# Optimization experiments

Measured on AMD Instinct MI355X. Metric: run time of the kernel, lower is better.

## Reference

```python
import jax, jax.numpy as jnp
import numpy as np

T, K, F = 131072, 64, 8
EPS = 1e-10


def setup_inputs() -> dict:
    key = jax.random.key(0)
    k0, k1, k2, k3 = jax.random.split(key, 4)
    return {
        "observations": jax.random.normal(k0, (T, F), dtype=jnp.float32),
        "beta_logits": jax.random.normal(k1, (K,), dtype=jnp.float32),
        "pi_logits": jax.random.normal(k2, (K, K), dtype=jnp.float32),
        "means": 0.1 * jax.random.normal(k3, (K, F), dtype=jnp.float32),
        "log_vars": jnp.zeros((K, F), dtype=jnp.float32),
    }


def _stick_breaking(logits):
    betas = jax.nn.sigmoid(logits)
    cp = jnp.cumprod(1.0 - betas)
    return betas * jnp.concatenate([jnp.ones((1,), betas.dtype), cp[:-1]])


def _emission_log_probs(obs, means, log_vars):
    # Diagonal-covariance MVN log-prob, vectorized over (T, K) via matmuls
    # logN(x; mu, diag(v)) = -0.5 * (sum((x-mu)^2/v) + sum(log v) + F*log(2pi))
    inv_var = jnp.exp(-log_vars)                                 # (K, F)
    quad = (obs ** 2) @ inv_var.T                                # (T, K): sum x^2/v
    cross = obs @ (means * inv_var).T                            # (T, K): sum x*mu/v
    const = jnp.sum(means ** 2 * inv_var + log_vars, axis=1)     # (K,)
    log2pi = jnp.float32(np.log(2.0 * np.pi))
    Fdim = obs.shape[1]
    return -0.5 * (quad - 2.0 * cross + const[None, :] + Fdim * log2pi)


def reference(observations, beta_logits, pi_logits, means, log_vars):
    beta_w = _stick_breaking(beta_logits)                        # (K,)
    trans = jax.nn.softmax(pi_logits, axis=1)                    # (K, K)
    em = jnp.exp(_emission_log_probs(observations, means, log_vars))  # (T, K)

    # Forward recursion
    a0 = beta_w * em[0]
    a0 = a0 / (a0.sum() + EPS)

    def fwd_step(a, e):
        a = (a @ trans) * e
        a = a / (a.sum() + EPS)
        return a, a

    _, alpha_rest = jax.lax.scan(fwd_step, a0, em[1:])
    alpha = jnp.concatenate([a0[None, :], alpha_rest], axis=0)   # (T, K)

    # Backward recursion: beta[t] = normalize(trans @ (beta[t+1] * em[t+1]))
    bT = jnp.ones((trans.shape[0],), observations.dtype)

    def bwd_step(b, e_next):
        b = trans @ (b * e_next)
        b = b / (b.sum() + EPS)
        return b, b

    _, beta_rev = jax.lax.scan(bwd_step, bT, em[1:], reverse=True)
    beta = jnp.concatenate([beta_rev, bT[None, :]], axis=0)      # (T, K)

    log_likelihood = jnp.log(alpha[-1].sum() + EPS)
    return alpha, beta, log_likelihood
```

## Files before the change

kernel.cpp:

```cpp
#include <hip/hip_runtime.h>

#define T_N   131072
#define K_N   64
#define L_C   64
#define F_N   8
#define N_CH  (T_N / L_C)
#define WARM  32
#define EPS_F 1e-10f
#define OBS_MAX ((T_N - 1) * F_N)

#define LOG2E 1.4426950408889634f
#define NL2E  (-0.72134752044448170f)
#define LN2   0.6931471805599453f
#define LN2PI 1.8378770664093453f
#define EMSC  16.0f

typedef float v2f __attribute__((ext_vector_type(2)));
typedef unsigned uint2v __attribute__((ext_vector_type(2)));

#define DPPI(SRC, CTRL) __builtin_amdgcn_update_dpp(0, (SRC), (CTRL), 0xF, 0xF, true)
#define DPPF(SRC, CTRL) __int_as_float(DPPI(__float_as_int(SRC), (CTRL)))

template <int CTRL>
__device__ __forceinline__ float dpp_add(float x) {
  int y = __builtin_amdgcn_update_dpp(0, __float_as_int(x), CTRL, 0xF, 0xF, true);
  return x + __int_as_float(y);
}
__device__ __forceinline__ float wave_sum64(float x) {
  x = dpp_add<0x111>(x);
  x = dpp_add<0x112>(x);
  x = dpp_add<0x114>(x);
  x = dpp_add<0x118>(x);
  x = dpp_add<0x142>(x);
  x = dpp_add<0x143>(x);
  return __int_as_float(__builtin_amdgcn_readlane(__float_as_int(x), 63));
}

#if __has_builtin(__builtin_amdgcn_permlane16_swap) && \
    __has_builtin(__builtin_amdgcn_permlane32_swap)
__device__ __forceinline__ float psum16(float x) {
  uint2v r = __builtin_amdgcn_permlane16_swap(__float_as_uint(x),
                                              __float_as_uint(x), false, false);
  return __uint_as_float(r.x) + __uint_as_float(r.y);
}
__device__ __forceinline__ float psum32(float x) {
  uint2v r = __builtin_amdgcn_permlane32_swap(__float_as_uint(x),
                                              __float_as_uint(x), false, false);
  return __uint_as_float(r.x) + __uint_as_float(r.y);
}
#else
__device__ __forceinline__ float psum16(float x) {
  return x + __int_as_float(
      __builtin_amdgcn_ds_swizzle(__float_as_int(x), 0x401F));
}
__device__ __forceinline__ float psum32(float x) {
  int addr = (((int)threadIdx.x ^ 32) & 63) << 2;
  return x + __int_as_float(
      __builtin_amdgcn_ds_bpermute(addr, __float_as_int(x)));
}
#endif

#define PKFMA(a, b, c) __builtin_elementwise_fma(a, b, c)

__device__ __forceinline__ float em_pk(const float4& xa, const float4& xb,
                                       const v2f civ2[4], const v2f cmiv2[4],
                                       float cc) {
  v2f x0 = {xa.x, xa.y}, x1 = {xa.z, xa.w};
  v2f x2 = {xb.x, xb.y}, x3 = {xb.z, xb.w};
  v2f a0 = {cc, 0.f}, a1 = {0.f, 0.f};
  a0 = PKFMA(x0, PKFMA(x0, civ2[0], cmiv2[0]), a0);
  a1 = PKFMA(x1, PKFMA(x1, civ2[1], cmiv2[1]), a1);
  a0 = PKFMA(x2, PKFMA(x2, civ2[2], cmiv2[2]), a0);
  a1 = PKFMA(x3, PKFMA(x3, civ2[3], cmiv2[3]), a1);
  v2f s = a0 + a1;
  return __builtin_amdgcn_exp2f(s.x + s.y);
}

#define MATVEC(VV, MOUT)                                                      \
  {                                                                           \
    float Gr[16];                                                             \
    Gr[0] = (VV);                                                             \
    Gr[1] = DPPF(Gr[0], 0xB1);                                 \
    Gr[2] = DPPF(Gr[0], 0x4E);                                 \
    Gr[3] = DPPF(Gr[1], 0x4E);                                                \
    _Pragma("unroll")                                                         \
    for (int rr = 0; rr < 4; ++rr) Gr[4 + rr] = DPPF(Gr[rr], 0x124);          \
    _Pragma("unroll")                                                         \
    for (int rr = 0; rr < 8; ++rr) Gr[8 + rr] = DPPF(Gr[rr], 0x128);          \
    v2f aE0 = {0.f,0.f}, aE1 = {0.f,0.f}, aO0 = {0.f,0.f}, aO1 = {0.f,0.f};   \
    _Pragma("unroll")                                                         \
    for (int rr = 0; rr < 8; ++rr) {                                          \
      v2f gg = {Gr[rr], Gr[rr]};                                              \
      aE0 = PKFMA(gg, TcE[rr], aE0);                                          \
      aO0 = PKFMA(gg, TcO[rr], aO0);                                          \
    }                                                                         \
    _Pragma("unroll")                                                         \
    for (int rr = 8; rr < 16; ++rr) {                                         \
      v2f gg = {Gr[rr], Gr[rr]};                                              \
      aE1 = PKFMA(gg, TcE[rr], aE1);                                          \
      aO1 = PKFMA(gg, TcO[rr], aO1);                                          \
    }                                                                         \
    v2f accE = aE0 + aE1, accO = aO0 + aO1;           \
    float pe0 = psum32(accE.x), pe2 = psum32(accE.y);                         \
    float po1 = psum32(accO.x), po3 = psum32(accO.y);                         \
    pe0 = psum16(pe0); pe2 = psum16(pe2);                                     \
    po1 = psum16(po1); po3 = psum16(po3);                                     \
    float tE = qb1 ? pe2 : pe0;                                               \
    float tO = qb1 ? po3 : po1;                                               \
    MOUT = qb0 ? tO : tE;                                                     \
  }

extern "C" __global__ void __launch_bounds__(64, 4)
hdphmm_fb(const float* __restrict__ obs,
          const float* __restrict__ beta_logits,
          const float* __restrict__ pi_logits,
          const float* __restrict__ means,
          const float* __restrict__ log_vars,
          float* __restrict__ out) {
  const int lane = threadIdx.x;
  const int bid  = blockIdx.x;
  const int h    = lane & 15;
  const bool qb0 = (lane >> 4) & 1;
  const bool qb1 = (lane >> 5) & 1;

  __shared__ __align__(8) float2 sstat[K_N];
  __shared__ float sb[K_N];

  float* alpha   = out;
  float* betaout = out + (size_t)T_N * K_N;

  v2f civ2[4], cmiv2[4];
  float c0, cw;
  {
    const float4* mp = reinterpret_cast<const float4*>(means + lane * F_N);
    const float4* lp = reinterpret_cast<const float4*>(log_vars + lane * F_N);
    float4 m0 = mp[0], m1 = mp[1];
    float4 l0 = lp[0], l1 = lp[1];
    float mu[8] = {m0.x, m0.y, m0.z, m0.w, m1.x, m1.y, m1.z, m1.w};
    float lv[8] = {l0.x, l0.y, l0.z, l0.w, l1.x, l1.y, l1.z, l1.w};
    float cst = F_N * LN2PI;
#pragma unroll
    for (int f = 0; f < 8; ++f) {
      float iv = __builtin_amdgcn_exp2f(-lv[f] * LOG2E);
      cst += lv[f] + mu[f] * mu[f] * iv;
      float cf  = NL2E * iv;
      civ2[f >> 1][f & 1]  = cf;
      cmiv2[f >> 1][f & 1] = -2.0f * mu[f] * cf;
    }
    c0 = NL2E * cst;
    cw = c0 + EMSC;
  }

  {
    const float4* pr4 = reinterpret_cast<const float4*>(pi_logits + lane * K_N);
    float mx = -3.0e38f;
#pragma unroll
    for (int k = 0; k < 16; ++k) {
      float4 r = pr4[k];
      mx = fmaxf(mx, fmaxf(fmaxf(r.x, r.y), fmaxf(r.z, r.w)));
    }
    float s = 0.0f;
#pragma unroll
    for (int k = 0; k < 16; ++k) {
      float4 r = pr4[k];
      s += __builtin_amdgcn_exp2f((r.x - mx) * LOG2E);
      s += __builtin_amdgcn_exp2f((r.y - mx) * LOG2E);
      s += __builtin_amdgcn_exp2f((r.z - mx) * LOG2E);
      s += __builtin_amdgcn_exp2f((r.w - mx) * LOG2E);
    }
    sstat[lane] = make_float2(mx, __builtin_amdgcn_rcpf(s));
  }
  __syncthreads();

  int ki[16];
  ki[0] = lane;
  ki[1] = DPPI(ki[0], 0xB1);
  ki[2] = DPPI(ki[0], 0x4E);
  ki[3] = DPPI(ki[1], 0x4E);
#pragma unroll
  for (int rr = 0; rr < 4; ++rr) ki[4 + rr] = DPPI(ki[rr], 0x124);
#pragma unroll
  for (int rr = 0; rr < 8; ++rr) ki[8 + rr] = DPPI(ki[rr], 0x128);

  v2f TcE[16], TcO[16];

  if (bid < N_CH) {
#pragma unroll
    for (int rr = 0; rr < 16; ++rr) {
      int k = ki[rr];
      float2 st = sstat[k];
      const float* pk = pi_logits + k * K_N;
      float e0 = __builtin_amdgcn_exp2f((pk[h]      - st.x) * LOG2E) * st.y;
      float e1 = __builtin_amdgcn_exp2f((pk[h + 16] - st.x) * LOG2E) * st.y;
      float e2 = __builtin_amdgcn_exp2f((pk[h + 32] - st.x) * LOG2E) * st.y;
      float e3 = __builtin_amdgcn_exp2f((pk[h + 48] - st.x) * LOG2E) * st.y;
      TcE[rr] = (v2f){e0, e2};
      TcO[rr] = (v2f){e1, e3};
    }

    const int out_lo = bid * L_C;
    float v;
    int t_first;
    if (bid == 0) {
      float bl = beta_logits[lane];
      float ex = __builtin_amdgcn_exp2f(-bl * LOG2E);
      float bw = __builtin_amdgcn_rcpf(1.0f + ex);
      sb[lane] = 1.0f - bw;
      __syncthreads();
      float pr = 1.0f;
#pragma unroll
      for (int i = 0; i < 64; ++i) {
        float qv = sb[i];
        pr = (i < lane) ? pr * qv : pr;
      }
      float4 x0 = reinterpret_cast<const float4*>(obs)[0];
      float4 x1 = reinterpret_cast<const float4*>(obs)[1];
      v = bw * pr * em_pk(x0, x1, civ2, cmiv2, c0);
      t_first = 1;
    } else {
      const int t0 = out_lo - WARM;
      const float4* xp = reinterpret_cast<const float4*>(obs + t0 * F_N);
      v = em_pk(xp[0], xp[1], civ2, cmiv2, cw);
      t_first = t0 + 1;
    }
    int obs_off = t_first * F_N;
    float4 xa, xb;
    {
      const float4* xp = reinterpret_cast<const float4*>(obs + obs_off);
      xa = xp[0]; xb = xp[1];
    }
    int out_off = out_lo * K_N + lane;

    const int wn8 = (bid == 0) ? 0 : (WARM >> 3);
#pragma unroll 1
    for (int o = 0; o < wn8; ++o) {
#pragma unroll
      for (int i = 0; i < 8; ++i) {
        float4 nxa = *reinterpret_cast<const float4*>(obs + obs_off + F_N);
        float4 nxb = *reinterpret_cast<const float4*>(obs + obs_off + F_N + 4);
        float m;
        MATVEC(v, m)
        float e = em_pk(xa, xb, civ2, cmiv2, cw);
        v = m * e;
        xa = nxa; xb = nxb; obs_off += F_N;
      }
      float Sw = wave_sum64(v);
      v *= __builtin_amdgcn_rcpf(Sw);
    }

    float S = wave_sum64(v);
    float r_st = __builtin_amdgcn_rcpf(S + EPS_F);

#define FWD_SSTEP                                                             \
  {                                                                           \
    int offn = obs_off + F_N; offn = (offn > OBS_MAX) ? OBS_MAX : offn;       \
    float4 nxa = *reinterpret_cast<const float4*>(obs + offn);                \
    float4 nxb = *reinterpret_cast<const float4*>(obs + offn + 4);            \
    float m;                                                                  \
    MATVEC(v, m)                                                              \
    alpha[out_off] = v * r_st; out_off += K_N;                                \
    float e = em_pk(xa, xb, civ2, cmiv2, c0);                                 \
    float vn = m * (r_st * e);                                                \
    S = wave_sum64(vn);                                                       \
    r_st = __builtin_amdgcn_rcpf(S + EPS_F);                                  \
    v = vn; xa = nxa; xb = nxb; obs_off = offn;                               \
  }

#pragma unroll 2
    for (int it = 0; it < L_C - 1; ++it) FWD_SSTEP
#undef FWD_SSTEP
    alpha[out_off] = v * r_st;
    if (bid == N_CH - 1 && lane == 0) {
      float sl = S * r_st + EPS_F;
      out[(size_t)2 * T_N * K_N] = __builtin_amdgcn_logf(sl) * LN2;
    }
  } else {
    {
      float2 s0 = sstat[h], s1 = sstat[h + 16];
      float2 s2 = sstat[h + 32], s3 = sstat[h + 48];
#pragma unroll
      for (int rr = 0; rr < 16; ++rr) {
        int k = ki[rr];
        float p0 = pi_logits[h * K_N + k];
        float p1 = pi_logits[(h + 16) * K_N + k];
        float p2 = pi_logits[(h + 32) * K_N + k];
        float p3 = pi_logits[(h + 48) * K_N + k];
        TcE[rr] = (v2f){__builtin_amdgcn_exp2f((p0 - s0.x) * LOG2E) * s0.y,
                        __builtin_amdgcn_exp2f((p2 - s2.x) * LOG2E) * s2.y};
        TcO[rr] = (v2f){__builtin_amdgcn_exp2f((p1 - s1.x) * LOG2E) * s1.y,
                        __builtin_amdgcn_exp2f((p3 - s3.x) * LOG2E) * s3.y};
      }
    }

    const int cb   = bid - N_CH;
    const int t_lo = cb * L_C;
    const int t_hi = t_lo + L_C - 1;
    int t_top = t_hi + WARM;
    if (t_top > T_N - 1) t_top = T_N - 1;
    const int s_top = (cb == N_CH - 1) ? T_N - 2 : t_hi;

    float w;
    {
      const float4* xp = reinterpret_cast<const float4*>(obs + t_top * F_N);
      w = em_pk(xp[0], xp[1], civ2, cmiv2, cw);
    }
    if (cb == N_CH - 1)
      betaout[(size_t)(T_N - 1) * K_N + lane] = 1.0f;
    int obs_off = (t_top - 1) * F_N;
    float4 xa, xb;
    {
      const float4* xp = reinterpret_cast<const float4*>(obs + obs_off);
      xa = xp[0]; xb = xp[1];
    }
    int out_off = s_top * K_N + lane;

#define BWD_WSTEP                                                             \
  {                                                                           \
    float4 nxa = *reinterpret_cast<const float4*>(obs + obs_off - F_N);       \
    float4 nxb = *reinterpret_cast<const float4*>(obs + obs_off - F_N + 4);   \
    float m;                                                                  \
    MATVEC(w, m)                                                              \
    float e = em_pk(xa, xb, civ2, cmiv2, cw);                                 \
    w = m * e;                                                                \
    xa = nxa; xb = nxb; obs_off -= F_N;                                       \
  }

    const int pw  = (t_top - s_top) - 1;
    const int pw8 = pw >> 3, pwr = pw & 7;
#pragma unroll 1
    for (int o = 0; o < pw8; ++o) {
#pragma unroll
      for (int i = 0; i < 8; ++i) BWD_WSTEP
      float Sw = wave_sum64(w);
      w *= __builtin_amdgcn_rcpf(Sw);
    }
#pragma unroll 1
    for (int it = 0; it < pwr; ++it) BWD_WSTEP
#undef BWD_WSTEP

    float u, S, r_st;
    {
      float m;
      MATVEC(w, m)
      float Sm = wave_sum64(m);
      u = m * __builtin_amdgcn_rcpf(Sm);
      float e = em_pk(xa, xb, civ2, cmiv2, c0);
      w = u * e;
      S = wave_sum64(u);
      r_st = __builtin_amdgcn_rcpf(S + EPS_F);
      int offn = obs_off - F_N; offn = (offn < 0) ? 0 : offn;
      xa = *reinterpret_cast<const float4*>(obs + offn);
      xb = *reinterpret_cast<const float4*>(obs + offn + 4);
      obs_off = offn;
    }

#define BWD_SSTEP                                                             \
  {                                                                           \
    int offn = obs_off - F_N; offn = (offn < 0) ? 0 : offn;                   \
    float4 nxa = *reinterpret_cast<const float4*>(obs + offn);                \
    float4 nxb = *reinterpret_cast<const float4*>(obs + offn + 4);            \
    float m;                                                                  \
    MATVEC(w, m)                                                              \
    betaout[out_off] = u * r_st; out_off -= K_N;                              \
    float u2 = m * r_st;                                                      \
    float e = em_pk(xa, xb, civ2, cmiv2, c0);                                 \
    w = u2 * e;                                                               \
    S = wave_sum64(u2);                                                       \
    r_st = __builtin_amdgcn_rcpf(S + EPS_F);                                  \
    u = u2; xa = nxa; xb = nxb; obs_off = offn;                               \
  }

    const int store_n = s_top - t_lo;
#pragma unroll 2
    for (int it = 0; it < store_n; ++it) BWD_SSTEP
#undef BWD_SSTEP
    betaout[t_lo * K_N + lane] = u * r_st;
  }
}

extern "C" void kernel_launch(void* const* d_in, const int* in_sizes, int n_in,
                              void* d_out, int out_size, void* d_ws, size_t ws_size,
                              hipStream_t stream) {
  (void)in_sizes; (void)n_in; (void)out_size; (void)d_ws; (void)ws_size;
  const float* obs  = (const float*)d_in[0];
  const float* bl   = (const float*)d_in[1];
  const float* pi   = (const float*)d_in[2];
  const float* mns  = (const float*)d_in[3];
  const float* lvs  = (const float*)d_in[4];
  hipLaunchKernelGGL(hdphmm_fb, dim3(2 * N_CH), dim3(64), 0, stream,
                     obs, bl, pi, mns, lvs, (float*)d_out);
}
```

Baseline: 174.1 us.

## Restructure per-step matvec into XOR-quadrant layout with fewer cross-lane reductions

Rearranges the register-held transition matrix so each lane holds entries for rows lane^16d, with gathered neighbour values packed pairwise. The matvec then produces four partial sums reduced with two psum16 and one psum32 instead of four psum32 plus four psum16 and select logic. This shortens the serial cross-lane reduction chain on every forward/backward step. Launch bounds occupancy hint is lowered from 4 to 2 waves, allowing more registers.

```diff
diff --git a/kernel.cpp b/kernel.cpp
--- a/kernel.cpp
+++ b/kernel.cpp
@@ -61,6 +61,7 @@
 #endif
 
 #define PKFMA(a, b, c) __builtin_elementwise_fma(a, b, c)
+#define RCP(x) __builtin_amdgcn_rcpf(x)
 
 __device__ __forceinline__ float em_pk(const float4& xa, const float4& xb,
                                        const v2f civ2[4], const v2f cmiv2[4],
@@ -80,37 +81,42 @@
   {                                                                           \
     float Gr[16];                                                             \
     Gr[0] = (VV);                                                             \
-    Gr[1] = DPPF(Gr[0], 0xB1);                                 \
-    Gr[2] = DPPF(Gr[0], 0x4E);                                 \
+    Gr[1] = DPPF(Gr[0], 0xB1);                                                \
+    Gr[2] = DPPF(Gr[0], 0x4E);                                                \
     Gr[3] = DPPF(Gr[1], 0x4E);                                                \
     _Pragma("unroll")                                                         \
     for (int rr = 0; rr < 4; ++rr) Gr[4 + rr] = DPPF(Gr[rr], 0x124);          \
     _Pragma("unroll")                                                         \
     for (int rr = 0; rr < 8; ++rr) Gr[8 + rr] = DPPF(Gr[rr], 0x128);          \
-    v2f aE0 = {0.f,0.f}, aE1 = {0.f,0.f}, aO0 = {0.f,0.f}, aO1 = {0.f,0.f};   \
+    v2f g_[8];                                                                \
     _Pragma("unroll")                                                         \
-    for (int rr = 0; rr < 8; ++rr) {                                          \
-      v2f gg = {Gr[rr], Gr[rr]};                                              \
-      aE0 = PKFMA(gg, TcE[rr], aE0);                                          \
-      aO0 = PKFMA(gg, TcO[rr], aO0);                                          \
+    for (int j_ = 0; j_ < 8; ++j_) g_[j_] = (v2f){Gr[2 * j_], Gr[2 * j_ + 1]};\
+    float X0_, X1_, X2_, X3_;                                                 \
+    _Pragma("unroll")                                                         \
+    for (int d_ = 0; d_ < 4; ++d_) {                                          \
+      v2f aA_ = {0.f, 0.f}, aB_ = {0.f, 0.f};                                 \
+      aA_ = PKFMA(g_[0], Tq[d_][0], aA_);                                     \
+      aB_ = PKFMA(g_[1], Tq[d_][1], aB_);                                     \
+      aA_ = PKFMA(g_[2], Tq[d_][2], aA_);                                     \
+      aB_ = PKFMA(g_[3], Tq[d_][3], aB_);                                     \
+      aA_ = PKFMA(g_[4], Tq[d_][4], aA_);                                     \
+      aB_ = PKFMA(g_[5], Tq[d_][5], aB_);                                     \
+      aA_ = PKFMA(g_[6], Tq[d_][6], aA_);                                     \
+      aB_ = PKFMA(g_[7], Tq[d_][7], aB_);                                     \
+      v2f s_ = aA_ + aB_;                                                     \
+      float xs_ = s_.x + s_.y;                                                \
+      if (d_ == 0) X0_ = xs_;                                                 \
+      else if (d_ == 1) X1_ = xs_;                                            \
+      else if (d_ == 2) X2_ = xs_;                                            \
+      else X3_ = xs_;                                                         \
     }                                                                         \
-    _Pragma("unroll")                                                         \
-    for (int rr = 8; rr < 16; ++rr) {                                         \
-      v2f gg = {Gr[rr], Gr[rr]};                                              \
-      aE1 = PKFMA(gg, TcE[rr], aE1);                                          \
-      aO1 = PKFMA(gg, TcO[rr], aO1);                                          \
-    }                                                                         \
-    v2f accE = aE0 + aE1, accO = aO0 + aO1;           \
-    float pe0 = psum32(accE.x), pe2 = psum32(accE.y);                         \
-    float po1 = psum32(accO.x), po3 = psum32(accO.y);                         \
-    pe0 = psum16(pe0); pe2 = psum16(pe2);                                     \
-    po1 = psum16(po1); po3 = psum16(po3);                                     \
-    float tE = qb1 ? pe2 : pe0;                                               \
-    float tO = qb1 ? po3 : po1;                                               \
-    MOUT = qb0 ? tO : tE;                                                     \
-  }
-
-extern "C" __global__ void __launch_bounds__(64, 4)
+    float e1_ = psum16(X1_) - X1_;                              \
+    float R_  = X2_ + (psum16(X3_) - X3_);                 \
+    float e2_ = psum32(R_) - R_;                     \
+    MOUT = (X0_ + e1_) + e2_;                                                 \
+  }
+
+extern "C" __global__ void __launch_bounds__(64, 2)
 hdphmm_fb(const float* __restrict__ obs,
           const float* __restrict__ beta_logits,
           const float* __restrict__ pi_logits,
@@ -119,9 +125,6 @@
           float* __restrict__ out) {
   const int lane = threadIdx.x;
   const int bid  = blockIdx.x;
-  const int h    = lane & 15;
-  const bool qb0 = (lane >> 4) & 1;
-  const bool qb1 = (lane >> 5) & 1;
 
   __shared__ __align__(8) float2 sstat[K_N];
   __shared__ float sb[K_N];
@@ -168,7 +171,7 @@
       s += __builtin_amdgcn_exp2f((r.z - mx) * LOG2E);
       s += __builtin_amdgcn_exp2f((r.w - mx) * LOG2E);
     }
-    sstat[lane] = make_float2(mx, __builtin_amdgcn_rcpf(s));
+    sstat[lane] = make_float2(mx, RCP(s));
   }
   __syncthreads();
 
@@ -182,20 +185,21 @@
 #pragma unroll
   for (int rr = 0; rr < 8; ++rr) ki[8 + rr] = DPPI(ki[rr], 0x128);
 
-  v2f TcE[16], TcO[16];
+  v2f Tq[4][8];
 
   if (bid < N_CH) {
 #pragma unroll
-    for (int rr = 0; rr < 16; ++rr) {
-      int k = ki[rr];
-      float2 st = sstat[k];
-      const float* pk = pi_logits + k * K_N;
-      float e0 = __builtin_amdgcn_exp2f((pk[h]      - st.x) * LOG2E) * st.y;
-      float e1 = __builtin_amdgcn_exp2f((pk[h + 16] - st.x) * LOG2E) * st.y;
-      float e2 = __builtin_amdgcn_exp2f((pk[h + 32] - st.x) * LOG2E) * st.y;
-      float e3 = __builtin_amdgcn_exp2f((pk[h + 48] - st.x) * LOG2E) * st.y;
-      TcE[rr] = (v2f){e0, e2};
-      TcO[rr] = (v2f){e1, e3};
+    for (int j = 0; j < 8; ++j) {
+      int k0 = ki[2 * j], k1 = ki[2 * j + 1];
+      float2 s0 = sstat[k0], s1 = sstat[k1];
+#pragma unroll
+      for (int d = 0; d < 4; ++d) {
+        int row = lane ^ (16 * d);
+        float p0 = pi_logits[(size_t)k0 * K_N + row];
+        float p1 = pi_logits[(size_t)k1 * K_N + row];
+        Tq[d][j] = (v2f){__builtin_amdgcn_exp2f((p0 - s0.x) * LOG2E) * s0.y,
+                         __builtin_amdgcn_exp2f((p1 - s1.x) * LOG2E) * s1.y};
+      }
     }
 
     const int out_lo = bid * L_C;
@@ -204,7 +208,7 @@
     if (bid == 0) {
       float bl = beta_logits[lane];
       float ex = __builtin_amdgcn_exp2f(-bl * LOG2E);
-      float bw = __builtin_amdgcn_rcpf(1.0f + ex);
+      float bw = RCP(1.0f + ex);
       sb[lane] = 1.0f - bw;
       __syncthreads();
       float pr = 1.0f;
@@ -245,11 +249,11 @@
         xa = nxa; xb = nxb; obs_off += F_N;
       }
       float Sw = wave_sum64(v);
-      v *= __builtin_amdgcn_rcpf(Sw);
+      v *= RCP(Sw);
     }
 
     float S = wave_sum64(v);
-    float r_st = __builtin_amdgcn_rcpf(S + EPS_F);
+    float r_st = RCP(S + EPS_F);
 
 #define FWD_SSTEP                                                             \
   {                                                                           \
@@ -262,7 +266,7 @@
     float e = em_pk(xa, xb, civ2, cmiv2, c0);                                 \
     float vn = m * (r_st * e);                                                \
     S = wave_sum64(vn);                                                       \
-    r_st = __builtin_amdgcn_rcpf(S + EPS_F);                                  \
+    r_st = RCP(S + EPS_F);                                                    \
     v = vn; xa = nxa; xb = nxb; obs_off = offn;                               \
   }
 
@@ -275,20 +279,17 @@
       out[(size_t)2 * T_N * K_N] = __builtin_amdgcn_logf(sl) * LN2;
     }
   } else {
-    {
-      float2 s0 = sstat[h], s1 = sstat[h + 16];
-      float2 s2 = sstat[h + 32], s3 = sstat[h + 48];
-#pragma unroll
-      for (int rr = 0; rr < 16; ++rr) {
-        int k = ki[rr];
-        float p0 = pi_logits[h * K_N + k];
-        float p1 = pi_logits[(h + 16) * K_N + k];
-        float p2 = pi_logits[(h + 32) * K_N + k];
-        float p3 = pi_logits[(h + 48) * K_N + k];
-        TcE[rr] = (v2f){__builtin_amdgcn_exp2f((p0 - s0.x) * LOG2E) * s0.y,
-                        __builtin_amdgcn_exp2f((p2 - s2.x) * LOG2E) * s2.y};
-        TcO[rr] = (v2f){__builtin_amdgcn_exp2f((p1 - s1.x) * LOG2E) * s1.y,
-                        __builtin_amdgcn_exp2f((p3 - s3.x) * LOG2E) * s3.y};
+#pragma unroll
+    for (int d = 0; d < 4; ++d) {
+      int row = lane ^ (16 * d);
+      float2 st = sstat[row];
+      const float* rp = pi_logits + (size_t)row * K_N;
+#pragma unroll
+      for (int j = 0; j < 8; ++j) {
+        float p0 = rp[ki[2 * j]];
+        float p1 = rp[ki[2 * j + 1]];
+        Tq[d][j] = (v2f){__builtin_amdgcn_exp2f((p0 - st.x) * LOG2E) * st.y,
+                         __builtin_amdgcn_exp2f((p1 - st.x) * LOG2E) * st.y};
       }
     }
 
@@ -332,7 +333,7 @@
 #pragma unroll
       for (int i = 0; i < 8; ++i) BWD_WSTEP
       float Sw = wave_sum64(w);
-      w *= __builtin_amdgcn_rcpf(Sw);
+      w *= RCP(Sw);
     }
 #pragma unroll 1
     for (int it = 0; it < pwr; ++it) BWD_WSTEP
@@ -343,11 +344,11 @@
       float m;
       MATVEC(w, m)
       float Sm = wave_sum64(m);
-      u = m * __builtin_amdgcn_rcpf(Sm);
+      u = m * RCP(Sm);
       float e = em_pk(xa, xb, civ2, cmiv2, c0);
       w = u * e;
       S = wave_sum64(u);
-      r_st = __builtin_amdgcn_rcpf(S + EPS_F);
+      r_st = RCP(S + EPS_F);
       int offn = obs_off - F_N; offn = (offn < 0) ? 0 : offn;
       xa = *reinterpret_cast<const float4*>(obs + offn);
       xb = *reinterpret_cast<const float4*>(obs + offn + 4);
@@ -366,7 +367,7 @@
     float e = em_pk(xa, xb, civ2, cmiv2, c0);                                 \
     w = u2 * e;                                                               \
     S = wave_sum64(u2);                                                       \
-    r_st = __builtin_amdgcn_rcpf(S + EPS_F);                                  \
+    r_st = RCP(S + EPS_F);                                                    \
     u = u2; xa = nxa; xb = nxb; obs_off = offn;                               \
   }
 
```

After: 160.3 us. 7.9% less time.
